# Kernel optimization log

Hardware: AMD Instinct MI355X
Metric: run time of the kernel (lower is better)

Reference implementation:

```python
import jax, jax.numpy as jnp
import numpy as np

B, S, V, E, H = 32, 64, 32000, 300, 1024


def setup_inputs() -> dict:
    key = jax.random.key(0)
    ks = jax.random.split(key, 16)
    s = 0.05
    inp = {
        "sent": jax.random.randint(ks[0], (B, S), 0, V),
        "length": jax.random.randint(ks[1], (B,), 2, S + 1),
        "emb": jax.random.normal(ks[2], (V, E), jnp.float32) * s,
        # layer 0: input E -> H ; layer 1: H -> H. PyTorch GRUCell layout [3H, in].
        "Wi0": jax.random.normal(ks[3], (3 * H, E), jnp.float32) * s,
        "Wh0": jax.random.normal(ks[4], (3 * H, H), jnp.float32) * s,
        "bi0": jnp.zeros((3 * H,), jnp.float32),
        "bh0": jnp.zeros((3 * H,), jnp.float32),
        "Wi1": jax.random.normal(ks[5], (3 * H, H), jnp.float32) * s,
        "Wh1": jax.random.normal(ks[6], (3 * H, H), jnp.float32) * s,
        "bi1": jnp.zeros((3 * H,), jnp.float32),
        "bh1": jnp.zeros((3 * H,), jnp.float32),
        "Wout": jax.random.normal(ks[7], (V, H), jnp.float32) * s,
        "bout": jnp.zeros((V,), jnp.float32),
    }
    return inp


def gru_step(x, h, Wi, Wh, bi, bh):
    gx = x @ Wi.T + bi            # [B, 3H]
    gh = h @ Wh.T + bh            # [B, 3H]
    rx, zx, nx = jnp.split(gx, 3, axis=-1)
    rh, zh, nh = jnp.split(gh, 3, axis=-1)
    r = jax.nn.sigmoid(rx + rh)
    z = jax.nn.sigmoid(zx + zh)
    n = jnp.tanh(nx + r * nh)
    return (1.0 - z) * n + z * h


def reference(sent, length, emb, Wi0, Wh0, bi0, bh0, Wi1, Wh1, bi1, bh1, Wout, bout):
    x = emb[sent]                              # [B, S, E]
    xs = jnp.swapaxes(x[:, : S - 1], 0, 1)     # [S-1, B, E]

    def step(carry, x_t):
        h0, h1 = carry
        h0 = gru_step(x_t, h0, Wi0, Wh0, bi0, bh0)
        h1 = gru_step(h0, h1, Wi1, Wh1, bi1, bh1)
        return (h0, h1), h1

    h_init = (jnp.zeros((B, H), x.dtype), jnp.zeros((B, H), x.dtype))
    _, hs = jax.lax.scan(step, h_init, xs)     # hs: [S-1, B, H]

    logits = jnp.einsum("sbh,vh->bsv", hs, Wout) + bout   # [B, S-1, V]
    logp = jax.nn.log_softmax(logits, axis=-1)
    targets = sent[:, 1:]                                   # [B, S-1]
    tok_logp = jnp.take_along_axis(logp, targets[:, :, None], axis=2)[..., 0]
    len_ng = length - 1                                     # [B]
    mask = jnp.arange(S - 1)[None, :] < len_ng[:, None]
    tok_logp = tok_logp * mask.astype(tok_logp.dtype)
    loss_batch = -jnp.sum(tok_logp, axis=1) / len_ng.astype(tok_logp.dtype)
    loss = jnp.mean(loss_batch)
    return loss, logits
```

## Files before the change

### kernel.cpp

```cpp
#include <hip/hip_runtime.h>

typedef unsigned short u16;
typedef unsigned int u32;
typedef unsigned long long u64;
typedef _Float16 f16;
typedef __attribute__((ext_vector_type(8))) __bf16 bf16x8;
typedef __attribute__((ext_vector_type(8))) _Float16 f16x8;
typedef __attribute__((ext_vector_type(4))) _Float16 f16x4;
typedef __attribute__((ext_vector_type(4))) float f32x4;

#define DEVI static __device__ __forceinline__

#define BB 32
#define SS 64
#define TT 63
#define VV 32000
#define EE 300
#define EP 320
#define HH 1024
#define H3 3072
#define MM 2016
#define MP 2048
#define NWG 192
#define NWG_TOT 256

DEVI u16 f2bf(float f) {
  u32 x = __float_as_uint(f);
  u32 r = x + 0x7FFFu + ((x >> 16) & 1u);
  return (u16)(r >> 16);
}
DEVI float bf2f(u16 h) { return __uint_as_float(((u32)h) << 16); }
DEVI float sigm(float x) { return 1.0f / (1.0f + __expf(-x)); }
DEVI float tanh_(float x) { return 2.0f / (1.0f + __expf(-2.0f * x)) - 1.0f; }

DEVI void gl_lds16(const void* g, void* l) {
  __builtin_amdgcn_global_load_lds((const __attribute__((address_space(1))) void*)g,
                                   (__attribute__((address_space(3))) void*)l,
                                   16, 0, 0);
}

DEVI f32x4 mfma_bf16(bf16x8 a, bf16x8 b, f32x4 c) {
  return __builtin_amdgcn_mfma_f32_16x16x32_bf16(a, b, c, 0, 0, 0);
}
DEVI f32x4 mfma_f16(f16x8 a, f16x8 b, f32x4 c) {
  return __builtin_amdgcn_mfma_f32_16x16x32_f16(a, b, c, 0, 0, 0);
}

DEVI f16x8 frag_ld(const f16* base, int kk, int kg, int brow) {
  const u64* q = (const u64*)base;
  int i0 = (kk * 8 + kg * 2) * 32 + brow;
  union { u64 u[2]; f16x8 v; } t;
  t.u[0] = __hip_atomic_load(q + i0, __ATOMIC_RELAXED, __HIP_MEMORY_SCOPE_AGENT);
  t.u[1] = __hip_atomic_load(q + i0 + 32, __ATOMIC_RELAXED, __HIP_MEMORY_SCOPE_AGENT);
  return t.v;
}
DEVI void ast32(u32* p, u32 v) {
  __hip_atomic_store(p, v, __ATOMIC_RELAXED, __HIP_MEMORY_SCOPE_AGENT);
}
DEVI u32 ald32(const u32* p) {
  return __hip_atomic_load(p, __ATOMIC_RELAXED, __HIP_MEMORY_SCOPE_AGENT);
}
DEVI u32* frag_wslot(f16* base, int j0, int b) {
  return (u32*)((char*)base + ((j0 >> 2) * 256 + b * 8 + (j0 & 3) * 2));
}

DEVI void gbar(u32* flags, int wg, u32 target) {
  __syncthreads();
  if (threadIdx.x == 0) ast32(&flags[wg * 16], target);
  int ok;
  do {
    u32 v = (threadIdx.x < NWG) ? ald32(&flags[threadIdx.x * 16]) : target;
    ok = (v >= target);
  } while (__syncthreads_and(ok) == 0);
}


__global__ void cvt3_f16(const float* __restrict__ s0, const float* __restrict__ s1,
                         const float* __restrict__ s2, f16* __restrict__ dst0) {
  const int seg = H3 * HH / 4;
  int i = blockIdx.x * 256 + threadIdx.x;
  int stride = gridDim.x * 256;
  for (; i < 3 * seg; i += stride) {
    int which = i / seg, off = i - which * seg;
    const float* s = (which == 0) ? s0 : (which == 1) ? s1 : s2;
    float4 v = ((const float4*)s)[off];
    f16x4 o = {(f16)v.x, (f16)v.y, (f16)v.z, (f16)v.w};
    ((f16x4*)dst0)[i] = o;
  }
}

__global__ void cvt_wi0_f16(const float* __restrict__ W, f16* __restrict__ out) {
  int i = blockIdx.x * 256 + threadIdx.x;
  int stride = gridDim.x * 256;
  for (; i < H3 * EP; i += stride) {
    int r = i / EP, c = i % EP;
    out[i] = (c < EE) ? (f16)W[(size_t)r * EE + c] : (f16)0.0f;
  }
}

__global__ void gather_x_f16(const int* __restrict__ sent, const float* __restrict__ emb,
                             f16* __restrict__ xf) {
  int i = blockIdx.x * 256 + threadIdx.x;
  int stride = gridDim.x * 256;
  for (; i < MM * EP; i += stride) {
    int m = i / EP, c = i % EP;
    int t = m >> 5, b = m & 31;
    int tok = sent[b * SS + t];
    xf[i] = (c < EE) ? (f16)emb[(size_t)tok * EE + c] : (f16)0.0f;
  }
}


template <bool REMAP, bool XSWZ>
__global__ __launch_bounds__(256) void gemm_bt(const u16* __restrict__ Ah, int lda,
                                               const u16* __restrict__ Bh,
                                               const float* __restrict__ bias,
                                               float* __restrict__ out, int out_stride,
                                               int Ksteps, int Mtiles, int Mvalid) {
  __shared__ u16 As[128 * 64];
  __shared__ u16 Bs[128 * 64];
  int bid = blockIdx.x;
  if (XSWZ) bid = (bid & 7) * (gridDim.x >> 3) + (bid >> 3);
  const int mtile = bid % Mtiles, ntile = bid / Mtiles;
  const int tid = threadIdx.x;
  const int lane = tid & 63, wave = tid >> 6;
  const int wrow = (wave & 1) * 64, wcol = (wave >> 1) * 64;
  const int l15 = lane & 15, kg = lane >> 4;

  f32x4 acc[4][4];
#pragma unroll
  for (int i = 0; i < 4; ++i)
#pragma unroll
    for (int j = 0; j < 4; ++j) {
      f32x4 z = {0.f, 0.f, 0.f, 0.f};
      acc[i][j] = z;
    }

  for (int ks = 0; ks < Ksteps; ++ks) {
    int k0 = ks * 64;
#pragma unroll
    for (int it = 0; it < 4; ++it) {
      int c = it * 256 + tid;
      int r = c >> 3, kc = (c & 7) * 8;
      gl_lds16(Ah + (size_t)(mtile * 128 + r) * lda + k0 + kc, &As[c * 8]);
      gl_lds16(Bh + (size_t)(ntile * 128 + r) * lda + k0 + kc, &Bs[c * 8]);
    }
    __syncthreads();
#pragma unroll
    for (int kk = 0; kk < 2; ++kk) {
      bf16x8 ah[4], bh[4];
#pragma unroll
      for (int i = 0; i < 4; ++i) {
        ah[i] = *(const bf16x8*)&As[(wrow + i * 16 + l15) * 64 + kk * 32 + kg * 8];
        bh[i] = *(const bf16x8*)&Bs[(wcol + i * 16 + l15) * 64 + kk * 32 + kg * 8];
      }
#pragma unroll
      for (int i = 0; i < 4; ++i)
#pragma unroll
        for (int j = 0; j < 4; ++j) acc[i][j] = mfma_bf16(ah[i], bh[j], acc[i][j]);
    }
    __syncthreads();
  }

  const int r0 = kg * 4;
#pragma unroll
  for (int i = 0; i < 4; ++i) {
    int mbase = mtile * 128 + wrow + i * 16 + r0;
#pragma unroll
    for (int j = 0; j < 4; ++j) {
      int n = ntile * 128 + wcol + j * 16 + l15;
      float bv = bias[n];
#pragma unroll
      for (int reg = 0; reg < 4; ++reg) {
        int m = mbase + reg;
        if (m < Mvalid) {
          float v = acc[i][j][reg] + bv;
          size_t oidx;
          if (REMAP) {
            int b = m & 31, s = m >> 5;
            oidx = ((size_t)(b * TT + s)) * VV + n;
          } else {
            oidx = (size_t)m * out_stride + n;
          }
          out[oidx] = v;
        }
      }
    }
  }
}

__global__ __launch_bounds__(256) void gemm_bt_f16(const f16* __restrict__ A, int lda,
                                                   const f16* __restrict__ B,
                                                   const float* __restrict__ bias,
                                                   float* __restrict__ out, int out_stride,
                                                   int Ksteps, int Mtiles, int Mvalid) {
  __shared__ f16 As[128 * 64];
  __shared__ f16 Bs[128 * 64];
  const int bid = blockIdx.x;
  const int mtile = bid % Mtiles, ntile = bid / Mtiles;
  const int tid = threadIdx.x;
  const int lane = tid & 63, wave = tid >> 6;
  const int wrow = (wave & 1) * 64, wcol = (wave >> 1) * 64;
  const int l15 = lane & 15, kg = lane >> 4;

  f32x4 acc[4][4];
#pragma unroll
  for (int i = 0; i < 4; ++i)
#pragma unroll
    for (int j = 0; j < 4; ++j) {
      f32x4 z = {0.f, 0.f, 0.f, 0.f};
      acc[i][j] = z;
    }

  for (int ks = 0; ks < Ksteps; ++ks) {
    int k0 = ks * 64;
#pragma unroll
    for (int it = 0; it < 4; ++it) {
      int c = it * 256 + tid;
      int r = c >> 3, kc = (c & 7) * 8;
      gl_lds16(A + (size_t)(mtile * 128 + r) * lda + k0 + kc, &As[c * 8]);
      gl_lds16(B + (size_t)(ntile * 128 + r) * lda + k0 + kc, &Bs[c * 8]);
    }
    __syncthreads();
#pragma unroll
    for (int kk = 0; kk < 2; ++kk) {
      f16x8 a[4], b[4];
#pragma unroll
      for (int i = 0; i < 4; ++i) {
        a[i] = *(const f16x8*)&As[(wrow + i * 16 + l15) * 64 + kk * 32 + kg * 8];
        b[i] = *(const f16x8*)&Bs[(wcol + i * 16 + l15) * 64 + kk * 32 + kg * 8];
      }
#pragma unroll
      for (int i = 0; i < 4; ++i)
#pragma unroll
        for (int j = 0; j < 4; ++j) acc[i][j] = mfma_f16(a[i], b[j], acc[i][j]);
    }
    __syncthreads();
  }

  const int r0 = kg * 4;
#pragma unroll
  for (int i = 0; i < 4; ++i) {
    int mbase = mtile * 128 + wrow + i * 16 + r0;
#pragma unroll
    for (int j = 0; j < 4; ++j) {
      int n = ntile * 128 + wcol + j * 16 + l15;
      float bv = bias[n];
#pragma unroll
      for (int reg = 0; reg < 4; ++reg) {
        int m = mbase + reg;
        if (m < Mvalid) {
          out[(size_t)m * out_stride + n] = acc[i][j][reg] + bv;
        }
      }
    }
  }
}


struct RecArgs {
  const f16 *wh0, *wi1, *wh1;
  const float *gx0, *bh0, *bi1, *bh1;
  f16 *h0x, *h1x;
  u16 *hs;
  u32 *bar;
  const float *wout;
  u16 *woutb;
};

__global__ __launch_bounds__(1024, 1) void rec_kernel(RecArgs ra) {
  __shared__ f16 wlds[48 * 1024];
  __shared__ float gh[4 * 48 * 33];
  const int tid = threadIdx.x;
  const int wg = blockIdx.x;

  if (wg >= NWG) {
    int i = (wg - NWG) * 1024 + tid;
    const int stride = (NWG_TOT - NWG) * 1024;
    for (; i < VV * HH / 4; i += stride) {
      float4 v = ((const float4*)ra.wout)[i];
      ushort4 o;
      o.x = f2bf(v.x); o.y = f2bf(v.y); o.z = f2bf(v.z); o.w = f2bf(v.w);
      ((ushort4*)ra.woutb)[i] = o;
    }
    return;
  }

  const int lane = tid & 63, wave = tid >> 6;
  const bool isL0 = wg < 64;
  const int Jbase = isL0 ? (wg * 16) : ((wg - 64) * 8);
  const int l15 = lane & 15;
  const int kg = lane >> 4;
  const int swz = (l15 & 7) << 4;
  const int kh = wave >> 2;
  const int khk = kh * 8;
  float* ghk = gh + kh * (48 * 33);
  char* wb = (char*)wlds;

#pragma unroll
  for (int it = 0; it < 6; ++it) {
    int q = it * 1024 + tid;
    int r = q >> 7;
    int c16 = q & 127;
    const f16* gp;
    if (isL0) {
      int gate = r >> 4, colr = r & 15;
      gp = ra.wh0 + ((size_t)(gate * HH + Jbase + colr)) * HH + c16 * 8;
    } else {
      int tile = r >> 3, colr = r & 7;
      int msrc = tile / 3, gate = tile - msrc * 3;
      const f16* W = msrc ? ra.wh1 : ra.wi1;
      gp = W + ((size_t)(gate * HH + Jbase + colr)) * HH + c16 * 8;
    }
    f16x8 v = *(const f16x8*)gp;
    int byte = r * 2048 + ((c16 * 16) ^ ((r & 7) << 4));
    *(f16x8*)(wb + byte) = v;
  }

  const int ewb = tid & 31, ewj = tid >> 5;
  float hprev = 0.f;
  float pb0r = 0.f, pb0z = 0.f, pb0n = 0.f;
  float pbrz_r = 0.f, pbrz_z = 0.f, pbn_i = 0.f, pbn_h = 0.f;
  if (isL0 && tid < 512) {
    int gj = Jbase + ewj;
    pb0r = ra.bh0[gj];
    pb0z = ra.bh0[HH + gj];
    pb0n = ra.bh0[2 * HH + gj];
  } else if (!isL0 && tid < 256) {
    int gj = Jbase + ewj;
    pbrz_r = ra.bi1[gj] + ra.bh1[gj];
    pbrz_z = ra.bi1[HH + gj] + ra.bh1[HH + gj];
    pbn_i = ra.bi1[2 * HH + gj];
    pbn_h = ra.bh1[2 * HH + gj];
  }
  __syncthreads();

  for (int p = 0; p < 64; ++p) {
    const int pb = p & 1, qb = (p + 1) & 1;
    if (isL0) {
      if (p < TT) {
        float gr = 0.f, gz = 0.f, gn = 0.f;
        if (tid < 512) {
          const float* gxb = ra.gx0 + ((size_t)p * BB + ewb) * H3;
          int gj = Jbase + ewj;
          gr = gxb[gj];
          gz = gxb[HH + gj];
          gn = gxb[2 * HH + gj];
        }
        const int rt = (wave >> 1) & 1, tt = wave & 1;
        const f16* h0base = ra.h0x + (size_t)qb * (BB * HH);
        const int brow = rt * 16 + l15;
        f32x4 z = {0.f, 0.f, 0.f, 0.f};
        if (tt == 0) {
          f32x4 acc0 = z, acc1 = z;
#pragma unroll 4
          for (int ki = 0; ki < 8; ++ki) {
            int kk = khk + ki;
            f16x8 a = frag_ld(h0base, kk, kg, brow);
            int inner = (kk * 64 + kg * 16) ^ swz;
            f16x8 b0 = *(const f16x8*)(wb + (0 * 16 + l15) * 2048 + inner);
            f16x8 b1 = *(const f16x8*)(wb + (1 * 16 + l15) * 2048 + inner);
            acc0 = mfma_f16(a, b0, acc0);
            acc1 = mfma_f16(a, b1, acc1);
          }
#pragma unroll
          for (int r = 0; r < 4; ++r) {
            ghk[(l15)*33 + rt * 16 + kg * 4 + r] = acc0[r];
            ghk[(16 + l15) * 33 + rt * 16 + kg * 4 + r] = acc1[r];
          }
        } else {
          f32x4 acc2 = z;
#pragma unroll 4
          for (int ki = 0; ki < 8; ++ki) {
            int kk = khk + ki;
            f16x8 a = frag_ld(h0base, kk, kg, brow);
            int inner = (kk * 64 + kg * 16) ^ swz;
            f16x8 b2 = *(const f16x8*)(wb + (2 * 16 + l15) * 2048 + inner);
            acc2 = mfma_f16(a, b2, acc2);
          }
#pragma unroll
          for (int r = 0; r < 4; ++r)
            ghk[(32 + l15) * 33 + rt * 16 + kg * 4 + r] = acc2[r];
        }
        __syncthreads();
        if (tid < 512) {
          f16* hxc = ra.h0x + (size_t)pb * (BB * HH);
          float rh = pb0r, zh = pb0z, nh = pb0n;
#pragma unroll
          for (int g = 0; g < 4; ++g) {
            rh += gh[g * (48 * 33) + (ewj)*33 + ewb];
            zh += gh[g * (48 * 33) + (16 + ewj) * 33 + ewb];
            nh += gh[g * (48 * 33) + (32 + ewj) * 33 + ewb];
          }
          float r = sigm(gr + rh);
          float zz = sigm(gz + zh);
          float n = tanh_(gn + r * nh);
          float hn = (1.f - zz) * n + zz * hprev;
          hprev = hn;
          float other = __shfl_xor(hn, 32);
          if ((lane & 32) == 0) {
            union { f16 h[2]; u32 u; } pk;
            pk.h[0] = (f16)hn;
            pk.h[1] = (f16)other;
            ast32(frag_wslot(hxc, Jbase + ewj, ewb), pk.u);
          }
        }
      } else {
        __syncthreads();
      }
    } else {
      if (p >= 1) {
        const int rt = (wave >> 1) & 1, src = wave & 1;
        const f16* hbase = (src ? ra.h1x : ra.h0x) + (size_t)qb * (BB * HH);
        const int brow = rt * 16 + l15;
        const int rowb = src * 24 + (l15 & 7);
        f32x4 z = {0.f, 0.f, 0.f, 0.f};
        f32x4 acc0 = z, acc1 = z, acc2 = z;
#pragma unroll 4
        for (int ki = 0; ki < 8; ++ki) {
          int kk = khk + ki;
          f16x8 a = frag_ld(hbase, kk, kg, brow);
          int inner = (kk * 64 + kg * 16) ^ swz;
          f16x8 b0 = *(const f16x8*)(wb + (rowb + 0) * 2048 + inner);
          f16x8 b1 = *(const f16x8*)(wb + (rowb + 8) * 2048 + inner);
          f16x8 b2 = *(const f16x8*)(wb + (rowb + 16) * 2048 + inner);
          acc0 = mfma_f16(a, b0, acc0);
          acc1 = mfma_f16(a, b1, acc1);
          acc2 = mfma_f16(a, b2, acc2);
        }
        if (l15 < 8) {
          f32x4 accs[3] = {acc0, acc1, acc2};
#pragma unroll
          for (int g = 0; g < 3; ++g) {
            int cl = (src * 3 + g) * 8 + l15;
#pragma unroll
            for (int r = 0; r < 4; ++r)
              ghk[cl * 33 + rt * 16 + kg * 4 + r] = accs[g][r];
          }
        }
        __syncthreads();
        if (tid < 256) {
          f16* hxc = ra.h1x + (size_t)pb * (BB * HH);
          float gir = 0.f, giz = 0.f, gin = 0.f, ghr = 0.f, ghz = 0.f, ghn = 0.f;
#pragma unroll
          for (int g = 0; g < 4; ++g) {
            const float* gg = gh + g * (48 * 33);
            gir += gg[(ewj)*33 + ewb];
            giz += gg[(8 + ewj) * 33 + ewb];
            gin += gg[(16 + ewj) * 33 + ewb];
            ghr += gg[(24 + ewj) * 33 + ewb];
            ghz += gg[(32 + ewj) * 33 + ewb];
            ghn += gg[(40 + ewj) * 33 + ewb];
          }
          float r = sigm(gir + ghr + pbrz_r);
          float zz = sigm(giz + ghz + pbrz_z);
          float n = tanh_(gin + pbn_i + r * (ghn + pbn_h));
          float hn = (1.f - zz) * n + zz * hprev;
          hprev = hn;
          float other = __shfl_xor(hn, 32);
          if ((lane & 32) == 0) {
            union { f16 h[2]; u32 u; } pk;
            pk.h[0] = (f16)hn;
            pk.h[1] = (f16)other;
            ast32(frag_wslot(hxc, Jbase + ewj, ewb), pk.u);
            union { u16 h[2]; u32 u; } pb2;
            pb2.h[0] = f2bf(hn);
            pb2.h[1] = f2bf(other);
            *(u32*)&ra.hs[((size_t)(p - 1) * BB + ewb) * HH + Jbase + ewj] = pb2.u;
          }
        }
      } else {
        __syncthreads();
      }
    }
    if (p < 63) gbar(ra.bar, wg, (u32)(p + 1));
  }
}


__global__ __launch_bounds__(256) void rowred_kernel(const float* __restrict__ logits,
                                                     const int* __restrict__ sent,
                                                     const int* __restrict__ length,
                                                     float* __restrict__ tok) {
  __shared__ float redm[4], reds[4];
  const int row = blockIdx.x;
  const int b = row / TT, s = row % TT;
  const float* p = logits + (size_t)row * VV;
  const int tid = threadIdx.x;
  const int lane = tid & 63, wave = tid >> 6;

  float m = -1e30f, sum = 0.f;
  for (int i = tid; i < VV; i += 256) {
    float v = p[i];
    if (v > m) {
      sum *= __expf(m - v);
      m = v;
    }
    sum += __expf(v - m);
  }
  for (int off = 1; off < 64; off <<= 1) {
    float mo = __shfl_xor(m, off);
    float so = __shfl_xor(sum, off);
    float mn = fmaxf(m, mo);
    sum = sum * __expf(m - mn) + so * __expf(mo - mn);
    m = mn;
  }
  if (lane == 0) {
    redm[wave] = m;
    reds[wave] = sum;
  }
  __syncthreads();
  if (tid == 0) {
    float M = redm[0], S = reds[0];
#pragma unroll
    for (int w = 1; w < 4; ++w) {
      float mo = redm[w], so = reds[w];
      float mn = fmaxf(M, mo);
      S = S * __expf(M - mn) + so * __expf(mo - mn);
      M = mn;
    }
    float lse = M + __logf(S);
    int tgt = sent[b * SS + s + 1];
    float tl = p[tgt] - lse;
    if (s >= length[b] - 1) tl = 0.f;
    tok[row] = tl;
  }
}

__global__ void loss_kernel(const float* __restrict__ tok, const int* __restrict__ length,
                            float* __restrict__ out0) {
  int lane = threadIdx.x;
  float v = 0.f;
  if (lane < BB) {
    float s = 0.f;
    for (int t = 0; t < TT; ++t) s += tok[lane * TT + t];
    float ln = (float)(length[lane] - 1);
    v = -s / ln;
  }
  v += __shfl_down(v, 16);
  v += __shfl_down(v, 8);
  v += __shfl_down(v, 4);
  v += __shfl_down(v, 2);
  v += __shfl_down(v, 1);
  if (lane == 0) out0[0] = v / (float)BB;
}


extern "C" void kernel_launch(void* const* d_in, const int* in_sizes, int n_in,
                              void* d_out, int out_size, void* d_ws, size_t ws_size,
                              hipStream_t stream) {
  const int* sent = (const int*)d_in[0];
  const int* length = (const int*)d_in[1];
  const float* emb = (const float*)d_in[2];
  const float* Wi0 = (const float*)d_in[3];
  const float* Wh0 = (const float*)d_in[4];
  const float* bi0 = (const float*)d_in[5];
  const float* bh0 = (const float*)d_in[6];
  const float* Wi1 = (const float*)d_in[7];
  const float* Wh1 = (const float*)d_in[8];
  const float* bi1 = (const float*)d_in[9];
  const float* bh1 = (const float*)d_in[10];
  const float* Wout = (const float*)d_in[11];
  const float* bout = (const float*)d_in[12];
  float* out = (float*)d_out;

  char* ws = (char*)d_ws;
  size_t off = 0;
  auto alloc = [&](size_t b) {
    char* p = ws + off;
    off = (off + b + 255) & ~(size_t)255;
    return p;
  };
  f16* wh0f = (f16*)alloc((size_t)H3 * HH * 2);
  f16* wi1f = (f16*)alloc((size_t)H3 * HH * 2);
  f16* wh1f = (f16*)alloc((size_t)H3 * HH * 2);
  f16* wi0f = (f16*)alloc((size_t)H3 * EP * 2);
  f16* xf = (f16*)alloc((size_t)MP * EP * 2);
  float* gx0 = (float*)alloc((size_t)MM * H3 * 4);
  u16* woutb = (u16*)alloc((size_t)VV * HH * 2);
  u16* hs = (u16*)alloc((size_t)MP * HH * 2);
  f16* h0x = (f16*)alloc((size_t)2 * BB * HH * 2);
  f16* h1x = (f16*)alloc((size_t)2 * BB * HH * 2);
  float* tok = (float*)alloc((size_t)MM * 4);
  u32* bar = (u32*)alloc((size_t)NWG * 16 * 4);

  hipMemsetAsync(h0x, 0, (size_t)2 * BB * HH * 2, stream);
  hipMemsetAsync(h1x, 0, (size_t)2 * BB * HH * 2, stream);
  hipMemsetAsync(hs, 0, (size_t)MP * HH * 2, stream);
  hipMemsetAsync(bar, 0, (size_t)NWG * 16 * 4, stream);
  hipMemsetAsync(xf + (size_t)MM * EP, 0, (size_t)(MP - MM) * EP * 2, stream);

  cvt3_f16<<<2048, 256, 0, stream>>>(Wh0, Wi1, Wh1, wh0f);
  cvt_wi0_f16<<<512, 256, 0, stream>>>(Wi0, wi0f);
  gather_x_f16<<<512, 256, 0, stream>>>(sent, emb, xf);

  gemm_bt_f16<<<16 * 24, 256, 0, stream>>>(xf, EP, wi0f, bi0, gx0, H3, 5, 16, MM);

  RecArgs ra{wh0f, wi1f, wh1f, gx0, bh0, bi1, bh1, h0x, h1x, hs, bar, Wout, woutb};
  void* kargs[] = {(void*)&ra};
  hipLaunchCooperativeKernel((void*)rec_kernel, dim3(NWG_TOT), dim3(1024), kargs, 0,
                             stream);

  gemm_bt<true, true><<<16 * 250, 256, 0, stream>>>(hs, HH, woutb, bout, out + 1, VV, 16,
                                                    16, MM);

  rowred_kernel<<<MM, 256, 0, stream>>>(out + 1, sent, length, tok);
  loss_kernel<<<1, 64, 0, stream>>>(tok, length, out);
}
```

Before: 785.1 us.

## Fuse partial log-softmax max/sum into output GEMM epilogue

The output projection GEMM now computes per-row running max and exp-sum for each 128-column tile in its epilogue and writes these partials to a small buffer. The row reduction kernel then combines 250 partials per row instead of re-reading the full logits row. This avoids a second full pass over the large logits tensor, at the cost of extra exp/shuffle work and shared memory in the GEMM epilogue.

Result: no change. 796.6 us (+1.5%).

```diff
diff --git a/kernel.cpp b/kernel.cpp
--- a/kernel.cpp
+++ b/kernel.cpp
@@ -23,6 +23,7 @@
 #define MP 2048
 #define NWG 192
 #define NWG_TOT 256
+#define NT 250
 
 DEVI u16 f2bf(float f) {
   u32 x = __float_as_uint(f);
@@ -116,9 +117,12 @@
                                                const u16* __restrict__ Bh,
                                                const float* __restrict__ bias,
                                                float* __restrict__ out, int out_stride,
-                                               int Ksteps, int Mtiles, int Mvalid) {
+                                               int Ksteps, int Mtiles, int Mvalid,
+                                               float* __restrict__ pmg,
+                                               float* __restrict__ psg) {
   __shared__ u16 As[128 * 64];
   __shared__ u16 Bs[128 * 64];
+  __shared__ float pm[128][2], ps[128][2];
   int bid = blockIdx.x;
   if (XSWZ) bid = (bid & 7) * (gridDim.x >> 3) + (bid >> 3);
   const int mtile = bid % Mtiles, ntile = bid / Mtiles;
@@ -184,6 +188,53 @@
           }
           out[oidx] = v;
         }
+      }
+    }
+  }
+
+  if constexpr (REMAP) {
+#pragma unroll
+    for (int i = 0; i < 4; ++i) {
+#pragma unroll
+      for (int reg = 0; reg < 4; ++reg) {
+        float rm = -1e30f, sm = 0.f;
+#pragma unroll
+        for (int j = 0; j < 4; ++j) {
+          int n = ntile * 128 + wcol + j * 16 + l15;
+          float v = acc[i][j][reg] + bias[n];
+          if (v > rm) {
+            sm *= __expf(rm - v);
+            rm = v;
+          }
+          sm += __expf(v - rm);
+        }
+#pragma unroll
+        for (int off = 1; off < 16; off <<= 1) {
+          float mo = __shfl_xor(rm, off);
+          float so = __shfl_xor(sm, off);
+          float mn = fmaxf(rm, mo);
+          sm = sm * __expf(rm - mn) + so * __expf(mo - mn);
+          rm = mn;
+        }
+        if (l15 == 0) {
+          int r128 = wrow + i * 16 + kg * 4 + reg;
+          pm[r128][wcol >> 6] = rm;
+          ps[r128][wcol >> 6] = sm;
+        }
+      }
+    }
+    __syncthreads();
+    if (tid < 128) {
+      int m = mtile * 128 + tid;
+      if (m < Mvalid) {
+        float m0 = pm[tid][0], m1 = pm[tid][1];
+        float s0 = ps[tid][0], s1 = ps[tid][1];
+        float mn = fmaxf(m0, m1);
+        float ss = s0 * __expf(m0 - mn) + s1 * __expf(m1 - mn);
+        int b = m & 31, s = m >> 5;
+        size_t rr = (size_t)(b * TT + s);
+        pmg[rr * NT + ntile] = mn;
+        psg[rr * NT + ntile] = ss;
       }
     }
   }
@@ -478,25 +529,22 @@
 }
 
 
-__global__ __launch_bounds__(256) void rowred_kernel(const float* __restrict__ logits,
-                                                     const int* __restrict__ sent,
-                                                     const int* __restrict__ length,
-                                                     float* __restrict__ tok) {
+__global__ __launch_bounds__(256) void rowred2_kernel(const float* __restrict__ pmg,
+                                                      const float* __restrict__ psg,
+                                                      const float* __restrict__ logits,
+                                                      const int* __restrict__ sent,
+                                                      const int* __restrict__ length,
+                                                      float* __restrict__ tok) {
   __shared__ float redm[4], reds[4];
   const int row = blockIdx.x;
   const int b = row / TT, s = row % TT;
-  const float* p = logits + (size_t)row * VV;
   const int tid = threadIdx.x;
   const int lane = tid & 63, wave = tid >> 6;
 
   float m = -1e30f, sum = 0.f;
-  for (int i = tid; i < VV; i += 256) {
-    float v = p[i];
-    if (v > m) {
-      sum *= __expf(m - v);
-      m = v;
-    }
-    sum += __expf(v - m);
+  if (tid < NT) {
+    m = pmg[(size_t)row * NT + tid];
+    sum = psg[(size_t)row * NT + tid];
   }
   for (int off = 1; off < 64; off <<= 1) {
     float mo = __shfl_xor(m, off);
@@ -521,7 +569,7 @@
     }
     float lse = M + __logf(S);
     int tgt = sent[b * SS + s + 1];
-    float tl = p[tgt] - lse;
+    float tl = logits[(size_t)row * VV + tgt] - lse;
     if (s >= length[b] - 1) tl = 0.f;
     tok[row] = tl;
   }
@@ -583,6 +631,8 @@
   f16* h1x = (f16*)alloc((size_t)2 * BB * HH * 2);
   float* tok = (float*)alloc((size_t)MM * 4);
   u32* bar = (u32*)alloc((size_t)NWG * 16 * 4);
+  float* pmg = (float*)alloc((size_t)MM * NT * 4);
+  float* psg = (float*)alloc((size_t)MM * NT * 4);
 
   hipMemsetAsync(h0x, 0, (size_t)2 * BB * HH * 2, stream);
   hipMemsetAsync(h1x, 0, (size_t)2 * BB * HH * 2, stream);
@@ -602,8 +652,8 @@
                              stream);
 
   gemm_bt<true, true><<<16 * 250, 256, 0, stream>>>(hs, HH, woutb, bout, out + 1, VV, 16,
-                                                    16, MM);
-
-  rowred_kernel<<<MM, 256, 0, stream>>>(out + 1, sent, length, tok);
+                                                    16, MM, pmg, psg);
+
+  rowred2_kernel<<<MM, 256, 0, stream>>>(pmg, psg, out + 1, sent, length, tok);
   loss_kernel<<<1, 64, 0, stream>>>(tok, length, out);
 }
```
